# Optimization experiments

Measured on AMD Instinct MI355X. Metric: run time of the kernel, lower is better.

Reference implementation:

```python
import jax, jax.numpy as jnp
import numpy as np

S, B, N, DIM = 64, 4, 256, 256
HEADS, DIM_HEAD = 8, 32
INNER = HEADS * DIM_HEAD  # 256
SCALE = DIM_HEAD ** -0.5
NEG = -1e10


def setup_inputs() -> dict:
    key = jax.random.key(0)
    k1, k2, k3, k4, k5 = jax.random.split(key, 5)
    x = jax.random.normal(k1, (S, B, N, DIM), dtype=jnp.float32)
    mask = jax.random.randint(k2, (S, N, N), 0, 2, dtype=jnp.int32)
    # nn.Linear(dim, inner*3, bias=False): y = x @ W_qkv  (W stored transposed)
    W_qkv = jax.random.normal(k3, (DIM, 3 * INNER), dtype=jnp.float32) / np.sqrt(DIM)
    W_out = jax.random.normal(k4, (INNER, DIM), dtype=jnp.float32) / np.sqrt(INNER)
    b_out = jax.random.normal(k5, (DIM,), dtype=jnp.float32) * 0.01
    return {"x": x, "mask": mask, "W_qkv": W_qkv, "W_out": W_out, "b_out": b_out}


def reference(x, mask, W_qkv, W_out, b_out):
    s, b, n, _ = x.shape
    qkv = x @ W_qkv                                  # [s,b,n,3*inner]
    q, k, v = jnp.split(qkv, 3, axis=-1)
    def to_heads(t):
        # s b n (h d) -> s b h n d
        return t.reshape(s, b, n, HEADS, DIM_HEAD).transpose(0, 1, 3, 2, 4)
    q, k, v = to_heads(q), to_heads(k), to_heads(v)
    sim = jnp.einsum('sbhid,sbhjd->sbhij', q, k) * SCALE
    sim = jnp.where(mask[:, None, None, :, :] == 0, NEG, sim)
    attn = jax.nn.softmax(sim, axis=-1)
    out = jnp.einsum('sbhij,sbhjd->sbhid', attn, v)
    out = out.transpose(0, 1, 3, 2, 4).reshape(s, b, n, INNER)  # s b h n d -> s b n (h d)
    return out @ W_out + b_out
```

## Files before the change

### kernel.cpp

```cpp
#include <hip/hip_runtime.h>

typedef __attribute__((ext_vector_type(8))) short bf16x8;
typedef __attribute__((ext_vector_type(4))) float f32x4;

__device__ __forceinline__ unsigned short f2bf(float f) {
  unsigned int u = __builtin_bit_cast(unsigned int, f);
  u += 0x7fffu + ((u >> 16) & 1u);
  return (unsigned short)(u >> 16);
}

__global__ __launch_bounds__(256) void cvt_kernel(const float* __restrict__ X,
                                                  unsigned short* __restrict__ Y) {
  const long long i = ((long long)blockIdx.x * 256 + threadIdx.x) * 8;
  float4 a = *reinterpret_cast<const float4*>(X + i);
  float4 b = *reinterpret_cast<const float4*>(X + i + 4);
  bf16x8 t;
  t[0] = (short)f2bf(a.x); t[1] = (short)f2bf(a.y);
  t[2] = (short)f2bf(a.z); t[3] = (short)f2bf(a.w);
  t[4] = (short)f2bf(b.x); t[5] = (short)f2bf(b.y);
  t[6] = (short)f2bf(b.z); t[7] = (short)f2bf(b.w);
  *reinterpret_cast<bf16x8*>(Y + i) = t;
}

template <bool C_F32>
__global__ __launch_bounds__(256) void gemm_kernel(
    const unsigned short* __restrict__ A,
    const float* __restrict__ B,
    void* __restrict__ Cv,
    const float* __restrict__ bias,
    int M, int N, int K)
{
  __shared__ __align__(16) unsigned short As[128][40];
  __shared__ __align__(16) unsigned short Bs[128][40];

  const int tid  = threadIdx.x;
  const int bm   = blockIdx.x * 128;
  const int bn   = blockIdx.y * 128;
  const int lane = tid & 63;
  const int wave = tid >> 6;
  const int wr   = (wave >> 1) * 64;
  const int wc   = (wave & 1) * 64;
  const int l15  = lane & 15;
  const int quad = lane >> 4;

  f32x4 acc[4][4];
#pragma unroll
  for (int r = 0; r < 4; ++r)
#pragma unroll
    for (int c = 0; c < 4; ++c) {
      f32x4 z = {0.f, 0.f, 0.f, 0.f};
      acc[r][c] = z;
    }

  const int ar   = tid >> 2;
  const int ac   = (tid & 3) * 8;
  const int bkr  = tid >> 3;
  const int bn16 = (tid & 7) * 16;

  for (int kk = 0; kk < K; kk += 32) {
    *reinterpret_cast<uint4*>(&As[ar][ac]) =
        *reinterpret_cast<const uint4*>(A + (size_t)(bm + ar) * K + kk + ac);
    *reinterpret_cast<uint4*>(&As[ar + 64][ac]) =
        *reinterpret_cast<const uint4*>(A + (size_t)(bm + ar + 64) * K + kk + ac);
    {
      const float* p = B + (size_t)(kk + bkr) * N + bn + bn16;
#pragma unroll
      for (int j = 0; j < 16; j += 4) {
        float4 f = *reinterpret_cast<const float4*>(p + j);
        Bs[bn16 + j + 0][bkr] = f2bf(f.x);
        Bs[bn16 + j + 1][bkr] = f2bf(f.y);
        Bs[bn16 + j + 2][bkr] = f2bf(f.z);
        Bs[bn16 + j + 3][bkr] = f2bf(f.w);
      }
    }
    __syncthreads();

    bf16x8 af[4], bf[4];
#pragma unroll
    for (int i = 0; i < 4; ++i) {
      af[i] = *reinterpret_cast<const bf16x8*>(&As[wr + i * 16 + l15][quad * 8]);
      bf[i] = *reinterpret_cast<const bf16x8*>(&Bs[wc + i * 16 + l15][quad * 8]);
    }
#pragma unroll
    for (int rt = 0; rt < 4; ++rt)
#pragma unroll
      for (int ct = 0; ct < 4; ++ct)
        acc[rt][ct] = __builtin_amdgcn_mfma_f32_16x16x32_bf16(af[rt], bf[ct], acc[rt][ct], 0, 0, 0);
    __syncthreads();
  }

#pragma unroll
  for (int rt = 0; rt < 4; ++rt)
#pragma unroll
    for (int ct = 0; ct < 4; ++ct)
#pragma unroll
      for (int i = 0; i < 4; ++i) {
        const int row = bm + wr + rt * 16 + quad * 4 + i;
        const int col = bn + wc + ct * 16 + l15;
        const float v = acc[rt][ct][i];
        if constexpr (C_F32) {
          ((float*)Cv)[(size_t)row * N + col] = v + bias[col];
        } else {
          ((unsigned short*)Cv)[(size_t)row * N + col] = f2bf(v);
        }
      }
}

#define SCALE_F 0.17677669529663689f

__global__ __launch_bounds__(256) void attn_kernel(
    const unsigned short* __restrict__ QKV,
    const int* __restrict__ mask,
    unsigned short* __restrict__ Aout)
{
  __shared__ __align__(16) unsigned short Ks[256 * 40];
  __shared__ __align__(16) unsigned short SH[4 * 16 * 280];

  const int blk  = blockIdx.x;
  const int h    = blk & 7;
  const int sb   = blk >> 3;
  const int s    = sb >> 2;
  const int t0   = sb << 8;
  const int tid  = threadIdx.x;
  const int lane = tid & 63;
  const int wave = tid >> 6;
  const int l15  = lane & 15;
  const int quad = lane >> 4;

  {
    const unsigned short* kp = QKV + (size_t)(t0 + tid) * 768 + 256 + h * 32;
    const unsigned short* vp = kp + 256;
    unsigned short* kd = Ks + tid * 40;
    unsigned short* vd = SH + tid * 40;
#pragma unroll
    for (int i = 0; i < 4; ++i) {
      *reinterpret_cast<uint4*>(kd + i * 8) = *reinterpret_cast<const uint4*>(kp + i * 8);
      *reinterpret_cast<uint4*>(vd + i * 8) = *reinterpret_cast<const uint4*>(vp + i * 8);
    }
  }
  __syncthreads();

  bf16x8 bv[2][8];
#pragma unroll
  for (int dt = 0; dt < 2; ++dt)
#pragma unroll
    for (int ks = 0; ks < 8; ++ks) {
      bf16x8 v;
#pragma unroll
      for (int j = 0; j < 8; ++j)
        v[j] = (short)SH[(ks * 32 + quad * 8 + j) * 40 + dt * 16 + l15];
      bv[dt][ks] = v;
    }
  __syncthreads();

  unsigned short* P = SH + wave * (16 * 280);

  for (int qb = 0; qb < 4; ++qb) {
    const int qbase = wave * 64 + qb * 16;

    bf16x8 qf = *reinterpret_cast<const bf16x8*>(
        QKV + (size_t)(t0 + qbase + l15) * 768 + h * 32 + quad * 8);

    f32x4 sim[16];
#pragma unroll
    for (int ct = 0; ct < 16; ++ct) {
      bf16x8 kf = *reinterpret_cast<const bf16x8*>(&Ks[(ct * 16 + l15) * 40 + quad * 8]);
      f32x4 z = {0.f, 0.f, 0.f, 0.f};
      sim[ct] = __builtin_amdgcn_mfma_f32_16x16x32_bf16(qf, kf, z, 0, 0, 0);
    }

    float lsum[4];
#pragma unroll
    for (int i = 0; i < 4; ++i) {
      const int qrow = qbase + quad * 4 + i;
      const int* mrow = mask + ((size_t)s * 256 + qrow) * 256 + l15;
      float mx = -3.0e38f;
#pragma unroll
      for (int ct = 0; ct < 16; ++ct) {
        float v = sim[ct][i] * SCALE_F;
        if (mrow[ct * 16] == 0) v = -1.0e10f;
        sim[ct][i] = v;
        mx = fmaxf(mx, v);
      }
#pragma unroll
      for (int off = 1; off < 16; off <<= 1)
        mx = fmaxf(mx, __shfl_xor(mx, off, 64));
      float sum = 0.f;
#pragma unroll
      for (int ct = 0; ct < 16; ++ct) {
        float e = __expf(sim[ct][i] - mx);
        sim[ct][i] = e;
        sum += e;
      }
#pragma unroll
      for (int off = 1; off < 16; off <<= 1)
        sum += __shfl_xor(sum, off, 64);
      lsum[i] = sum;
    }

#pragma unroll
    for (int i = 0; i < 4; ++i)
#pragma unroll
      for (int ct = 0; ct < 16; ++ct)
        P[(quad * 4 + i) * 280 + ct * 16 + l15] = f2bf(sim[ct][i]);
    __syncthreads();

    f32x4 o0 = {0.f, 0.f, 0.f, 0.f};
    f32x4 o1 = {0.f, 0.f, 0.f, 0.f};
#pragma unroll
    for (int ks = 0; ks < 8; ++ks) {
      bf16x8 pf = *reinterpret_cast<const bf16x8*>(&P[l15 * 280 + ks * 32 + quad * 8]);
      o0 = __builtin_amdgcn_mfma_f32_16x16x32_bf16(pf, bv[0][ks], o0, 0, 0, 0);
      o1 = __builtin_amdgcn_mfma_f32_16x16x32_bf16(pf, bv[1][ks], o1, 0, 0, 0);
    }

#pragma unroll
    for (int i = 0; i < 4; ++i) {
      const float rl = 1.0f / lsum[i];
      const size_t row = (size_t)t0 + qbase + quad * 4 + i;
      Aout[row * 256 + h * 32 + l15]      = f2bf(o0[i] * rl);
      Aout[row * 256 + h * 32 + 16 + l15] = f2bf(o1[i] * rl);
    }
    __syncthreads();
  }
}

extern "C" void kernel_launch(void* const* d_in, const int* in_sizes, int n_in,
                              void* d_out, int out_size, void* d_ws, size_t ws_size,
                              hipStream_t stream) {
  const float* X    = (const float*)d_in[0];
  const int*   mask = (const int*)d_in[1];
  const float* Wqkv = (const float*)d_in[2];
  const float* Wout = (const float*)d_in[3];
  const float* bout = (const float*)d_in[4];
  float*       outp = (float*)d_out;

  unsigned short* QKV  = (unsigned short*)d_ws;
  unsigned short* Xbf  = QKV + (size_t)65536 * 768;
  unsigned short* Amid = Xbf;

  dim3 blk(256);
  cvt_kernel<<<dim3(8192), blk, 0, stream>>>(X, Xbf);
  gemm_kernel<false><<<dim3(512, 6), blk, 0, stream>>>(Xbf, Wqkv, (void*)QKV, nullptr, 65536, 768, 256);
  attn_kernel<<<dim3(2048), blk, 0, stream>>>(QKV, mask, Amid);
  gemm_kernel<true><<<dim3(512, 2), blk, 0, stream>>>(Amid, Wout, (void*)outp, bout, 65536, 256, 256);
}
```

Baseline: 355.3 us.

## Pre-transpose weights to bf16 and stage GEMM tiles with global_load_lds

Adds a small kernel that converts and transposes each weight matrix to bf16 once per call, so the GEMM B operand is K-contiguous like A. The GEMM then loads both A and B tiles directly into LDS with 16-byte global_load_lds instead of per-element fp32 loads, bf16 conversion and strided LDS stores. The LDS tiles lose their row padding, which may cause bank conflicts on fragment reads. Scratch for the transposed weights is borrowed from the output buffer and the QKV region before they are written.

```diff
diff --git a/kernel.cpp b/kernel.cpp
--- a/kernel.cpp
+++ b/kernel.cpp
@@ -7,6 +7,12 @@
   unsigned int u = __builtin_bit_cast(unsigned int, f);
   u += 0x7fffu + ((u >> 16) & 1u);
   return (unsigned short)(u >> 16);
+}
+
+typedef const __attribute__((address_space(1))) unsigned int* as1_u32p;
+typedef __attribute__((address_space(3))) unsigned int* as3_u32p;
+__device__ __forceinline__ void glds16(const void* g, void* l) {
+  __builtin_amdgcn_global_load_lds((as1_u32p)g, (as3_u32p)l, 16, 0, 0);
 }
 
 __global__ __launch_bounds__(256) void cvt_kernel(const float* __restrict__ X,
@@ -22,16 +28,31 @@
   *reinterpret_cast<bf16x8*>(Y + i) = t;
 }
 
+__global__ __launch_bounds__(256) void transpose_bf16_kernel(
+    const float* __restrict__ S, unsigned short* __restrict__ D, int R, int C) {
+  __shared__ float T[32][33];
+  const int bx = blockIdx.x * 32;
+  const int by = blockIdx.y * 32;
+  const int tx = threadIdx.x & 31, ty = threadIdx.x >> 5;
+#pragma unroll
+  for (int k = 0; k < 4; ++k)
+    T[ty + 8 * k][tx] = S[(size_t)(by + ty + 8 * k) * C + bx + tx];
+  __syncthreads();
+#pragma unroll
+  for (int k = 0; k < 4; ++k)
+    D[(size_t)(bx + ty + 8 * k) * R + by + tx] = f2bf(T[tx][ty + 8 * k]);
+}
+
 template <bool C_F32>
-__global__ __launch_bounds__(256) void gemm_kernel(
+__global__ __launch_bounds__(256) void gemm_bt(
     const unsigned short* __restrict__ A,
-    const float* __restrict__ B,
+    const unsigned short* __restrict__ Bt,
     void* __restrict__ Cv,
     const float* __restrict__ bias,
     int M, int N, int K)
 {
-  __shared__ __align__(16) unsigned short As[128][40];
-  __shared__ __align__(16) unsigned short Bs[128][40];
+  __shared__ __align__(16) unsigned short As[128 * 32];
+  __shared__ __align__(16) unsigned short Bs[128 * 32];
 
   const int tid  = threadIdx.x;
   const int bm   = blockIdx.x * 128;
@@ -52,34 +73,27 @@
       acc[r][c] = z;
     }
 
-  const int ar   = tid >> 2;
-  const int ac   = (tid & 3) * 8;
-  const int bkr  = tid >> 3;
-  const int bn16 = (tid & 7) * 16;
+  const unsigned short* gA0 = A  + (size_t)(bm + wave * 16 + (lane >> 2)) * K + (lane & 3) * 8;
+  const unsigned short* gA1 = gA0 + (size_t)64 * K;
+  const unsigned short* gB0 = Bt + (size_t)(bn + wave * 16 + (lane >> 2)) * K + (lane & 3) * 8;
+  const unsigned short* gB1 = gB0 + (size_t)64 * K;
+  unsigned short* lA0 = As + wave * 512;
+  unsigned short* lA1 = As + 2048 + wave * 512;
+  unsigned short* lB0 = Bs + wave * 512;
+  unsigned short* lB1 = Bs + 2048 + wave * 512;
 
   for (int kk = 0; kk < K; kk += 32) {
-    *reinterpret_cast<uint4*>(&As[ar][ac]) =
-        *reinterpret_cast<const uint4*>(A + (size_t)(bm + ar) * K + kk + ac);
-    *reinterpret_cast<uint4*>(&As[ar + 64][ac]) =
-        *reinterpret_cast<const uint4*>(A + (size_t)(bm + ar + 64) * K + kk + ac);
-    {
-      const float* p = B + (size_t)(kk + bkr) * N + bn + bn16;
-#pragma unroll
-      for (int j = 0; j < 16; j += 4) {
-        float4 f = *reinterpret_cast<const float4*>(p + j);
-        Bs[bn16 + j + 0][bkr] = f2bf(f.x);
-        Bs[bn16 + j + 1][bkr] = f2bf(f.y);
-        Bs[bn16 + j + 2][bkr] = f2bf(f.z);
-        Bs[bn16 + j + 3][bkr] = f2bf(f.w);
-      }
-    }
+    glds16(gA0 + kk, lA0);
+    glds16(gA1 + kk, lA1);
+    glds16(gB0 + kk, lB0);
+    glds16(gB1 + kk, lB1);
     __syncthreads();
 
     bf16x8 af[4], bf[4];
 #pragma unroll
     for (int i = 0; i < 4; ++i) {
-      af[i] = *reinterpret_cast<const bf16x8*>(&As[wr + i * 16 + l15][quad * 8]);
-      bf[i] = *reinterpret_cast<const bf16x8*>(&Bs[wc + i * 16 + l15][quad * 8]);
+      af[i] = *reinterpret_cast<const bf16x8*>(&As[(wr + i * 16 + l15) * 32 + quad * 8]);
+      bf[i] = *reinterpret_cast<const bf16x8*>(&Bs[(wc + i * 16 + l15) * 32 + quad * 8]);
     }
 #pragma unroll
     for (int rt = 0; rt < 4; ++rt)
@@ -235,13 +249,19 @@
   const float* bout = (const float*)d_in[4];
   float*       outp = (float*)d_out;
 
-  unsigned short* QKV  = (unsigned short*)d_ws;
-  unsigned short* Xbf  = QKV + (size_t)65536 * 768;
-  unsigned short* Amid = Xbf;
+  unsigned short* QKV   = (unsigned short*)d_ws;
+  unsigned short* Xbf   = QKV + (size_t)65536 * 768;
+  unsigned short* Amid  = Xbf;
+  unsigned short* WoutT = QKV;
+  unsigned short* WqkvT = (unsigned short*)d_out;
 
   dim3 blk(256);
   cvt_kernel<<<dim3(8192), blk, 0, stream>>>(X, Xbf);
-  gemm_kernel<false><<<dim3(512, 6), blk, 0, stream>>>(Xbf, Wqkv, (void*)QKV, nullptr, 65536, 768, 256);
+  transpose_bf16_kernel<<<dim3(24, 8), blk, 0, stream>>>(Wqkv, WqkvT, 256, 768);
+
+  gemm_bt<false><<<dim3(512, 6), blk, 0, stream>>>(Xbf, WqkvT, (void*)QKV, nullptr, 65536, 768, 256);
   attn_kernel<<<dim3(2048), blk, 0, stream>>>(QKV, mask, Amid);
-  gemm_kernel<true><<<dim3(512, 2), blk, 0, stream>>>(Amid, Wout, (void*)outp, bout, 65536, 256, 256);
-}
+
+  transpose_bf16_kernel<<<dim3(8, 8), blk, 0, stream>>>(Wout, WoutT, 256, 256);
+  gemm_bt<true><<<dim3(512, 2), blk, 0, stream>>>(Amid, WoutT, (void*)outp, bout, 65536, 256, 256);
+}
```

Result: faster. 321.2 us (-9.6%).
